# Performance work log

Hardware: AMD Instinct MI355X
Metric: run time of the kernel (lower is better)

The kernel has to match this reference:

```python
import jax, jax.numpy as jnp
import numpy as np

# Complete 32-ary tree of depth 3: vocab = 32**3 = 32768 leaves.
B = 4096       # batch
NHID = 512     # hidden size
BR = 32        # branching factor (num_children at every internal node)
DEPTH = 3      # number of internal-node decisions from root to leaf
V = BR ** DEPTH
NUM_NODES = sum(BR ** k for k in range(DEPTH))  # 1 + 32 + 1024 = 1057

# Static tree-indexing tables (level-order node numbering).
_LEVEL_OFFSET = np.array([sum(BR ** j for j in range(k)) for k in range(DEPTH)], dtype=np.int64)   # [0, 1, 33]
_NODE_DIV = np.array([BR ** (DEPTH - k) for k in range(DEPTH)], dtype=np.int64)                    # node-within-level divisor
_STEP_DIV = np.array([BR ** (DEPTH - 1 - k) for k in range(DEPTH)], dtype=np.int64)                # child-step divisor


def setup_inputs() -> dict:
    key = jax.random.key(0)
    k1, k2, k3 = jax.random.split(key, 3)
    inputs = jax.random.normal(k1, (B, NHID), dtype=jnp.float32)
    labels = jax.random.randint(k2, (B,), 0, V)                     # leaf index per sample
    W = jax.random.normal(k3, (NUM_NODES, NHID, BR), dtype=jnp.float32)  # all node params, stacked
    return {"inputs": inputs, "labels": labels, "W": W}


def reference(inputs, labels, W):
    lab = labels[:, None]                                            # [B, 1]
    node_idx = jnp.asarray(_LEVEL_OFFSET)[None, :] + lab // jnp.asarray(_NODE_DIV)[None, :]  # [B, D] node on path
    steps = (lab // jnp.asarray(_STEP_DIV)[None, :]) % BR            # [B, D] child taken at each node
    Wg = W[node_idx]                                                 # [B, D, NHID, BR] gathered path params
    logits = jnp.einsum('bh,bdhc->bdc', inputs, Wg)                  # [B, D, BR]
    p = jax.nn.softmax(logits, axis=-1)
    step_p = jnp.take_along_axis(p, steps[:, :, None], axis=-1)[..., 0]  # [B, D]
    return jnp.prod(step_p, axis=-1)                                 # [B] path probability
```

## Files before the change

kernel.cpp:

```cpp
#include <hip/hip_runtime.h>


#define NHID  512
#define BR    32
#define BATCH 4096
#define NBUCK 1024
#define SMAX  8
#define GMAX  1536

#define FMA4(A, xv, wv_) do { \
    (A).x = fmaf((xv), (wv_).x, (A).x); \
    (A).y = fmaf((xv), (wv_).y, (A).y); \
    (A).z = fmaf((xv), (wv_).z, (A).z); \
    (A).w = fmaf((xv), (wv_).w, (A).w); } while (0)

__global__ __launch_bounds__(1024) void k_sort(const int* __restrict__ labels,
                                               int* __restrict__ order,
                                               int* __restrict__ ngroups,
                                               int* __restrict__ gdesc) {
    __shared__ int labs[BATCH];
    __shared__ int hist[NBUCK];
    __shared__ int wsum1[16];
    __shared__ int wsum2[16];
    const int t  = threadIdx.x;
    const int wv = t >> 6;
    const int ln = t & 63;

    hist[t] = 0;
    #pragma unroll
    for (int r = 0; r < BATCH / 1024; ++r)
        labs[t + 1024 * r] = labels[t + 1024 * r];
    __syncthreads();
    #pragma unroll
    for (int r = 0; r < BATCH / 1024; ++r)
        atomicAdd(&hist[labs[t + 1024 * r] >> 5], 1);
    __syncthreads();

    const int cnt  = hist[t];
    const int gcnt = (cnt + SMAX - 1) / SMAX;

    int s1 = cnt, s2 = gcnt;
    #pragma unroll
    for (int d = 1; d < 64; d <<= 1) {
        int u1 = __shfl_up(s1, d);
        int u2 = __shfl_up(s2, d);
        if (ln >= d) { s1 += u1; s2 += u2; }
    }
    if (ln == 63) { wsum1[wv] = s1; wsum2[wv] = s2; }
    __syncthreads();
    if (t < 16) {
        int a = wsum1[t], b = wsum2[t];
        #pragma unroll
        for (int d = 1; d < 16; d <<= 1) {
            int ua = __shfl_up(a, d, 16);
            int ub = __shfl_up(b, d, 16);
            if (t >= d) { a += ua; b += ub; }
        }
        wsum1[t] = a; wsum2[t] = b;
        if (t == 15) *ngroups = b;
    }
    __syncthreads();
    const int base1 = (wv > 0) ? wsum1[wv - 1] : 0;
    const int base2 = (wv > 0) ? wsum2[wv - 1] : 0;
    const int off  = base1 + s1 - cnt;
    const int goff = base2 + s2 - gcnt;
    hist[t] = off;
    __syncthreads();

    for (int j = 0; j < gcnt; ++j)
        gdesc[goff + j] = (off + j * SMAX)
                        | (min(SMAX, cnt - j * SMAX) << 12)
                        | (t << 16);

    #pragma unroll
    for (int r = 0; r < BATCH / 1024; ++r) {
        int j = t + 1024 * r;
        int pos = atomicAdd(&hist[labs[j] >> 5], 1);
        order[pos] = j;
    }
}

__global__ __launch_bounds__(192) void hsm_g8(
    const float* __restrict__ inputs,
    const int* __restrict__ labels,
    const float* __restrict__ W,
    const int* __restrict__ order,
    const int* __restrict__ ngroups,
    const int* __restrict__ gdesc,
    float* __restrict__ out)
{
    __shared__ float xsT[NHID * SMAX];
    __shared__ float pk[3][SMAX];
    __shared__ int   sids[SMAX];
    __shared__ int   slab[SMAX];

    const int gid = blockIdx.x;
    if (gid >= *ngroups) return;
    const int d     = gdesc[gid];
    const int start = d & 0xFFF;
    const int m     = (d >> 12) & 0xF;
    const int g     = d >> 16;
    const int tid   = threadIdx.x;

    if (tid < SMAX) {
        int sid = (tid < m) ? order[start + tid] : -1;
        sids[tid] = sid;
        slab[tid] = (sid >= 0) ? labels[sid] : 0;
    }
    __syncthreads();

    for (int h = tid; h < NHID; h += 192) {
        float v[SMAX];
        #pragma unroll
        for (int s = 0; s < SMAX; ++s) {
            int id = sids[s];
            v[s] = (id >= 0) ? inputs[(size_t)id * NHID + h] : 0.0f;
        }
        float4* dst = (float4*)&xsT[h * SMAX];
        dst[0] = make_float4(v[0], v[1], v[2], v[3]);
        dst[1] = make_float4(v[4], v[5], v[6], v[7]);
    }
    __syncthreads();

    const int k    = tid >> 6;
    const int lane = tid & 63;
    const int colg = lane & 7;
    const int hsel = lane >> 3;

    const int node = (k == 0) ? 0 : (k == 1) ? 1 + (g >> 5) : 33 + g;
    const int step01 = (k == 0) ? (g >> 5) : (g & 31);

    const float4* wp = (const float4*)(W + (size_t)node * (NHID * BR))
                       + hsel * 8 + colg;
    const float4* xp = (const float4*)xsT + hsel * 2;

    float4 acc[SMAX];
    #pragma unroll
    for (int s = 0; s < SMAX; ++s) acc[s] = make_float4(0, 0, 0, 0);

    #pragma unroll 8
    for (int i = 0; i < 64; ++i) {
        float4 w  = wp[i * 64];
        float4 xa = xp[i * 16];
        float4 xb = xp[i * 16 + 1];
        FMA4(acc[0], xa.x, w); FMA4(acc[1], xa.y, w);
        FMA4(acc[2], xa.z, w); FMA4(acc[3], xa.w, w);
        FMA4(acc[4], xb.x, w); FMA4(acc[5], xb.y, w);
        FMA4(acc[6], xb.z, w); FMA4(acc[7], xb.w, w);
    }

    #pragma unroll
    for (int s = 0; s < SMAX; ++s) {
        #pragma unroll
        for (int mm = 8; mm <= 32; mm <<= 1) {
            acc[s].x += __shfl_xor(acc[s].x, mm);
            acc[s].y += __shfl_xor(acc[s].y, mm);
            acc[s].z += __shfl_xor(acc[s].z, mm);
            acc[s].w += __shfl_xor(acc[s].w, mm);
        }
    }

    #pragma unroll
    for (int s = 0; s < SMAX; ++s) {
        float4 a = acc[s];
        float mx = fmaxf(fmaxf(a.x, a.y), fmaxf(a.z, a.w));
        #pragma unroll
        for (int mm = 1; mm <= 4; mm <<= 1) mx = fmaxf(mx, __shfl_xor(mx, mm));
        float es = expf(a.x - mx) + expf(a.y - mx) + expf(a.z - mx) + expf(a.w - mx);
        #pragma unroll
        for (int mm = 1; mm <= 4; mm <<= 1) es += __shfl_xor(es, mm);

        int step = (k == 2) ? (slab[s] & 31) : step01;
        int e = step & 3;
        float v = (e == 0) ? a.x : (e == 1) ? a.y : (e == 2) ? a.z : a.w;
        float sl = __shfl(v, step >> 2);
        float p = expf(sl - mx) / es;
        if (lane == 0) pk[k][s] = p;
    }
    __syncthreads();

    if (tid < SMAX && sids[tid] >= 0)
        out[sids[tid]] = pk[0][tid] * pk[1][tid] * pk[2][tid];
}

extern "C" void kernel_launch(void* const* d_in, const int* in_sizes, int n_in,
                              void* d_out, int out_size, void* d_ws, size_t ws_size,
                              hipStream_t stream)
{
    const float* inputs = (const float*)d_in[0];
    const int*   labels = (const int*)d_in[1];
    const float* W      = (const float*)d_in[2];
    float* out = (float*)d_out;

    char* ws = (char*)d_ws;
    int* order   = (int*)ws;
    int* ngroups = (int*)(ws + 16384);
    int* gdesc   = (int*)(ws + 16384 + 128);

    k_sort<<<dim3(1),    dim3(1024), 0, stream>>>(labels, order, ngroups, gdesc);
    hsm_g8<<<dim3(GMAX), dim3(192),  0, stream>>>(inputs, labels, W, order,
                                                  ngroups, gdesc, out);
}
```

Measured before the change: 126.2 us.

## Stream node weights into LDS with async global_load_lds double buffering

Each wave now copies its node's weight matrix into a per-wave double-buffered LDS region using the global-to-LDS DMA builtin, 1024 floats per chunk. It waits with s_waitcnt vmcnt so the next chunk's load overlaps the FMAs on the current chunk. The goal is to hide global-memory latency on the weight stream that was previously loaded straight into registers. The cost is 24 KB of extra LDS per block, which can lower occupancy, plus an extra LDS read per weight.

```diff
diff --git a/kernel.cpp b/kernel.cpp
--- a/kernel.cpp
+++ b/kernel.cpp
@@ -13,6 +13,19 @@
     (A).y = fmaf((xv), (wv_).y, (A).y); \
     (A).z = fmaf((xv), (wv_).z, (A).z); \
     (A).w = fmaf((xv), (wv_).w, (A).w); } while (0)
+
+__device__ __forceinline__ void dma16(const float* g, float* l) {
+    __builtin_amdgcn_global_load_lds(
+        (const __attribute__((address_space(1))) void*)g,
+        (__attribute__((address_space(3))) void*)l,
+        16, 0, 0);
+}
+__device__ __forceinline__ void wait_vm4() {
+    asm volatile("s_waitcnt vmcnt(4)" ::: "memory");
+}
+__device__ __forceinline__ void wait_vm0() {
+    asm volatile("s_waitcnt vmcnt(0)" ::: "memory");
+}
 
 __global__ __launch_bounds__(1024) void k_sort(const int* __restrict__ labels,
                                                int* __restrict__ order,
@@ -80,7 +93,7 @@
     }
 }
 
-__global__ __launch_bounds__(192) void hsm_g8(
+__global__ __launch_bounds__(192) void hsm_dma(
     const float* __restrict__ inputs,
     const int* __restrict__ labels,
     const float* __restrict__ W,
@@ -90,6 +103,7 @@
     float* __restrict__ out)
 {
     __shared__ float xsT[NHID * SMAX];
+    __shared__ float wlds[3 * 2 * 1024];
     __shared__ float pk[3][SMAX];
     __shared__ int   sids[SMAX];
     __shared__ int   slab[SMAX];
@@ -122,31 +136,50 @@
     }
     __syncthreads();
 
-    const int k    = tid >> 6;
+    const int wv   = tid >> 6;
     const int lane = tid & 63;
     const int colg = lane & 7;
     const int hsel = lane >> 3;
 
-    const int node = (k == 0) ? 0 : (k == 1) ? 1 + (g >> 5) : 33 + g;
-    const int step01 = (k == 0) ? (g >> 5) : (g & 31);
-
-    const float4* wp = (const float4*)(W + (size_t)node * (NHID * BR))
-                       + hsel * 8 + colg;
-    const float4* xp = (const float4*)xsT + hsel * 2;
+    const int node = (wv == 0) ? 0 : (wv == 1) ? 1 + (g >> 5) : 33 + g;
+    const int step01 = (wv == 0) ? (g >> 5) : (g & 31);
+
+    const float* wg = W + (size_t)node * (NHID * BR);
+    float* wb = &wlds[wv * 2048];
 
     float4 acc[SMAX];
     #pragma unroll
     for (int s = 0; s < SMAX; ++s) acc[s] = make_float4(0, 0, 0, 0);
 
-    #pragma unroll 8
-    for (int i = 0; i < 64; ++i) {
-        float4 w  = wp[i * 64];
-        float4 xa = xp[i * 16];
-        float4 xb = xp[i * 16 + 1];
-        FMA4(acc[0], xa.x, w); FMA4(acc[1], xa.y, w);
-        FMA4(acc[2], xa.z, w); FMA4(acc[3], xa.w, w);
-        FMA4(acc[4], xb.x, w); FMA4(acc[5], xb.y, w);
-        FMA4(acc[6], xb.z, w); FMA4(acc[7], xb.w, w);
+    #pragma unroll
+    for (int j = 0; j < 4; ++j)
+        dma16(wg + j * 256 + lane * 4, wb + j * 256);
+
+    #pragma unroll 4
+    for (int c = 0; c < 16; ++c) {
+        const float* cur = wb + (c & 1) * 1024;
+        float* nxt = wb + ((c + 1) & 1) * 1024;
+        if (c < 15) {
+            const float* gsrc = wg + (c + 1) * 1024;
+            #pragma unroll
+            for (int j = 0; j < 4; ++j)
+                dma16(gsrc + j * 256 + lane * 4, nxt + j * 256);
+            wait_vm4();
+        } else {
+            wait_vm0();
+        }
+        #pragma unroll
+        for (int t = 0; t < 4; ++t) {
+            const int rr = hsel + 8 * t;
+            float4 w = *(const float4*)&cur[rr * 32 + colg * 4];
+            const float4* xr = (const float4*)&xsT[(c * 32 + rr) * SMAX];
+            float4 xa = xr[0];
+            float4 xb = xr[1];
+            FMA4(acc[0], xa.x, w); FMA4(acc[1], xa.y, w);
+            FMA4(acc[2], xa.z, w); FMA4(acc[3], xa.w, w);
+            FMA4(acc[4], xb.x, w); FMA4(acc[5], xb.y, w);
+            FMA4(acc[6], xb.z, w); FMA4(acc[7], xb.w, w);
+        }
     }
 
     #pragma unroll
@@ -170,12 +203,12 @@
         #pragma unroll
         for (int mm = 1; mm <= 4; mm <<= 1) es += __shfl_xor(es, mm);
 
-        int step = (k == 2) ? (slab[s] & 31) : step01;
+        int step = (wv == 2) ? (slab[s] & 31) : step01;
         int e = step & 3;
         float v = (e == 0) ? a.x : (e == 1) ? a.y : (e == 2) ? a.z : a.w;
         float sl = __shfl(v, step >> 2);
         float p = expf(sl - mx) / es;
-        if (lane == 0) pk[k][s] = p;
+        if (lane == 0) pk[wv][s] = p;
     }
     __syncthreads();
 
@@ -197,7 +230,7 @@
     int* ngroups = (int*)(ws + 16384);
     int* gdesc   = (int*)(ws + 16384 + 128);
 
-    k_sort<<<dim3(1),    dim3(1024), 0, stream>>>(labels, order, ngroups, gdesc);
-    hsm_g8<<<dim3(GMAX), dim3(192),  0, stream>>>(inputs, labels, W, order,
-                                                  ngroups, gdesc, out);
-}
+    k_sort <<<dim3(1),    dim3(1024), 0, stream>>>(labels, order, ngroups, gdesc);
+    hsm_dma<<<dim3(GMAX), dim3(192),  0, stream>>>(inputs, labels, W, order,
+                                                   ngroups, gdesc, out);
+}
```

Measured after the change: 140.8 us. 11.6% more time.

## Split hidden-dim reduction across four waves per level with shared-memory combine

Applied to the files above, without the earlier changes.

Each block now runs 12 waves (768 threads) instead of 3: every tree level's 512-long dot product is split into four quarter-K slices, each handled by its own wave. Partial logits go to shared memory and are summed, then the softmax runs with 32-lane shuffles over the columns. The aim is more memory-level parallelism and a shorter serial loop per wave, hiding latency on the W gathers. The costs are extra shared memory, an additional block barrier, and register pressure from the 768-thread launch bound.

```diff
diff --git a/kernel.cpp b/kernel.cpp
--- a/kernel.cpp
+++ b/kernel.cpp
@@ -80,7 +80,7 @@
     }
 }
 
-__global__ __launch_bounds__(192) void hsm_g8(
+__global__ __launch_bounds__(768, 6) void hsm_w12(
     const float* __restrict__ inputs,
     const int* __restrict__ labels,
     const float* __restrict__ W,
@@ -90,6 +90,7 @@
     float* __restrict__ out)
 {
     __shared__ float xsT[NHID * SMAX];
+    __shared__ float partial[3 * 4 * SMAX * BR];
     __shared__ float pk[3][SMAX];
     __shared__ int   sids[SMAX];
     __shared__ int   slab[SMAX];
@@ -109,7 +110,8 @@
     }
     __syncthreads();
 
-    for (int h = tid; h < NHID; h += 192) {
+    if (tid < NHID) {
+        const int h = tid;
         float v[SMAX];
         #pragma unroll
         for (int s = 0; s < SMAX; ++s) {
@@ -122,31 +124,32 @@
     }
     __syncthreads();
 
-    const int k    = tid >> 6;
+    const int w    = tid >> 6;
     const int lane = tid & 63;
+    const int k    = w >> 2;
+    const int q    = w & 3;
     const int colg = lane & 7;
     const int hsel = lane >> 3;
 
     const int node = (k == 0) ? 0 : (k == 1) ? 1 + (g >> 5) : 33 + g;
-    const int step01 = (k == 0) ? (g >> 5) : (g & 31);
 
     const float4* wp = (const float4*)(W + (size_t)node * (NHID * BR))
-                       + hsel * 8 + colg;
-    const float4* xp = (const float4*)xsT + hsel * 2;
+                       + q * 1024 + hsel * 8 + colg;
+    const float4* xp = (const float4*)xsT + (128 * q + hsel) * 2;
 
     float4 acc[SMAX];
     #pragma unroll
     for (int s = 0; s < SMAX; ++s) acc[s] = make_float4(0, 0, 0, 0);
 
-    #pragma unroll 8
-    for (int i = 0; i < 64; ++i) {
-        float4 w  = wp[i * 64];
+    #pragma unroll
+    for (int i = 0; i < 16; ++i) {
+        float4 w4 = wp[i * 64];
         float4 xa = xp[i * 16];
         float4 xb = xp[i * 16 + 1];
-        FMA4(acc[0], xa.x, w); FMA4(acc[1], xa.y, w);
-        FMA4(acc[2], xa.z, w); FMA4(acc[3], xa.w, w);
-        FMA4(acc[4], xb.x, w); FMA4(acc[5], xb.y, w);
-        FMA4(acc[6], xb.z, w); FMA4(acc[7], xb.w, w);
+        FMA4(acc[0], xa.x, w4); FMA4(acc[1], xa.y, w4);
+        FMA4(acc[2], xa.z, w4); FMA4(acc[3], xa.w, w4);
+        FMA4(acc[4], xb.x, w4); FMA4(acc[5], xb.y, w4);
+        FMA4(acc[6], xb.z, w4); FMA4(acc[7], xb.w, w4);
     }
 
     #pragma unroll
@@ -159,23 +162,34 @@
             acc[s].w += __shfl_xor(acc[s].w, mm);
         }
     }
-
-    #pragma unroll
-    for (int s = 0; s < SMAX; ++s) {
-        float4 a = acc[s];
-        float mx = fmaxf(fmaxf(a.x, a.y), fmaxf(a.z, a.w));
-        #pragma unroll
-        for (int mm = 1; mm <= 4; mm <<= 1) mx = fmaxf(mx, __shfl_xor(mx, mm));
-        float es = expf(a.x - mx) + expf(a.y - mx) + expf(a.z - mx) + expf(a.w - mx);
-        #pragma unroll
-        for (int mm = 1; mm <= 4; mm <<= 1) es += __shfl_xor(es, mm);
-
-        int step = (k == 2) ? (slab[s] & 31) : step01;
-        int e = step & 3;
-        float v = (e == 0) ? a.x : (e == 1) ? a.y : (e == 2) ? a.z : a.w;
-        float sl = __shfl(v, step >> 2);
-        float p = expf(sl - mx) / es;
-        if (lane == 0) pk[k][s] = p;
+    if (lane < 8) {
+        #pragma unroll
+        for (int s = 0; s < SMAX; ++s)
+            *(float4*)&partial[((k * 4 + q) * SMAX + s) * BR + lane * 4] = acc[s];
+    }
+    __syncthreads();
+
+    {
+        const int kk  = tid >> 8;
+        const int s   = (tid >> 5) & 7;
+        const int col = tid & 31;
+        float l = 0.0f;
+        #pragma unroll
+        for (int qq = 0; qq < 4; ++qq)
+            l += partial[((kk * 4 + qq) * SMAX + s) * BR + col];
+        float mx = l;
+        #pragma unroll
+        for (int mm = 1; mm <= 16; mm <<= 1)
+            mx = fmaxf(mx, __shfl_xor(mx, mm, 32));
+        float e  = expf(l - mx);
+        float es = e;
+        #pragma unroll
+        for (int mm = 1; mm <= 16; mm <<= 1)
+            es += __shfl_xor(es, mm, 32);
+        int step = (kk == 0) ? (g >> 5)
+                 : (kk == 1) ? (g & 31)
+                             : (slab[s] & 31);
+        if (col == step) pk[kk][s] = e / es;
     }
     __syncthreads();
 
@@ -197,7 +211,7 @@
     int* ngroups = (int*)(ws + 16384);
     int* gdesc   = (int*)(ws + 16384 + 128);
 
-    k_sort<<<dim3(1),    dim3(1024), 0, stream>>>(labels, order, ngroups, gdesc);
-    hsm_g8<<<dim3(GMAX), dim3(192),  0, stream>>>(inputs, labels, W, order,
-                                                  ngroups, gdesc, out);
+    k_sort <<<dim3(1),    dim3(1024), 0, stream>>>(labels, order, ngroups, gdesc);
+    hsm_w12<<<dim3(GMAX), dim3(768),  0, stream>>>(inputs, labels, W, order,
+                                                   ngroups, gdesc, out);
 }
```

Measured after the change: 126.0 us. Within noise of the previous version (-0.2%).
